# Kernel tuning notes

Hardware: AMD Instinct MI355X
Metric: run time of the kernel (lower is better)

The kernel has to match this reference:

```python
import jax, jax.numpy as jnp
import numpy as np

N = 8192
D_IN = 6       # dim(concat(node, centre)) = 3 + 3
D_OUT = 512    # output_size


def setup_inputs() -> dict:
    key = jax.random.key(0)
    ks = jax.random.split(key, 9)
    s_in = 1.0 / np.sqrt(D_IN)
    s_v = 1.0 / np.sqrt(2 * D_OUT)
    return {
        "nodes": jax.random.normal(ks[0], (N, 3), dtype=jnp.float32),
        "centre": jax.random.normal(ks[1], (1, 3), dtype=jnp.float32),
        "Wq": jax.random.uniform(ks[2], (D_OUT, D_IN), jnp.float32, -s_in, s_in),
        "bq": jax.random.uniform(ks[3], (D_OUT,), jnp.float32, -s_in, s_in),
        "Wk": jax.random.uniform(ks[4], (D_OUT, D_IN), jnp.float32, -s_in, s_in),
        "bk": jax.random.uniform(ks[5], (D_OUT,), jnp.float32, -s_in, s_in),
        "Wv": jax.random.uniform(ks[6], (D_OUT, 2 * D_OUT), jnp.float32, -s_v, s_v),
        "bv": jax.random.uniform(ks[7], (D_OUT,), jnp.float32, -s_v, s_v),
    }


def reference(nodes, centre, Wq, bq, Wk, bk, Wv, bv):
    n = nodes.shape[0]
    d = Wv.shape[0]
    # x = concat(nodes, broadcast centre)  -> [N, 6]
    x = jnp.concatenate([nodes, jnp.broadcast_to(centre, (n, centre.shape[1]))], axis=1)
    keys = x @ Wk.T + bk          # [N, D]
    queries = x @ Wq.T + bq       # [N, D]
    attn = jax.nn.softmax(keys @ queries.T, axis=1)  # [N, N], rows sum to 1
    # values(concat(queries, keys[n])) decomposes linearly:
    #   V[n, m] = queries[m] @ Wv_q.T + keys[n] @ Wv_k.T + bv
    # so out[n] = attn[n] @ (queries @ Wv_q.T) + keys[n] @ Wv_k.T + bv
    Wv_q = Wv[:, :d]
    Wv_k = Wv[:, d:]
    out = attn @ (queries @ Wv_q.T) + keys @ Wv_k.T + bv
    return keys + out
```

## Files before the change

### kernel.cpp

```cpp
#include <hip/hip_runtime.h>

#define N_NODES 8192
#define DOUT    512
#define LOG2E   1.4426950408889634f
#define SQRT3   1.7320508075688772f

__device__ __forceinline__ float exp2_raw(float x) {
    float r;
    asm("v_exp_f32 %0, %1" : "=v"(r) : "v"(x));
    return r;
}


__global__ __launch_bounds__(128) void k2_tables_aux(
    const float* __restrict__ nodes, const float* __restrict__ centre,
    const float* __restrict__ Wq, const float* __restrict__ bq,
    const float* __restrict__ Wk, const float* __restrict__ bk,
    const float* __restrict__ Wv, const float* __restrict__ bv,
    float* __restrict__ T, float* __restrict__ aux)
{
    __shared__ float red[16];
    const int r = blockIdx.x, tid = threadIdx.x, lane = tid & 63, wv = tid >> 6;
    const float c0 = centre[0], c1 = centre[1], c2 = centre[2];

    if (r < 512) {
        const float* wvq = Wv + (size_t)r * 1024;
        const float* wvk = wvq + 512;

        float m0=0.f,m1=0.f,m2=0.f,uc=0.f,r0=0.f,r1=0.f,r2=0.f,rc=0.f;
        #pragma unroll
        for (int it = 0; it < 4; ++it) {
            int s = it*128 + tid;
            float a = wvq[s];
            float b = wvk[s];
            const float2* wk2 = (const float2*)(Wk + s*6);
            const float2* wq2 = (const float2*)(Wq + s*6);
            float2 k01 = wk2[0], k23 = wk2[1], k45 = wk2[2];
            float2 q01 = wq2[0], q23 = wq2[1], q45 = wq2[2];
            float kcs = fmaf(k23.y, c0, fmaf(k45.x, c1, fmaf(k45.y, c2, bk[s])));
            float us  = fmaf(q23.y, c0, fmaf(q45.x, c1, fmaf(q45.y, c2, bq[s])));
            m0 = fmaf(a, q01.x, m0);
            m1 = fmaf(a, q01.y, m1);
            m2 = fmaf(a, q23.x, m2);
            uc = fmaf(a, us, uc);
            r0 = fmaf(b, k01.x, r0);
            r1 = fmaf(b, k01.y, r1);
            r2 = fmaf(b, k23.x, r2);
            rc = fmaf(b, kcs, rc);
        }
        #pragma unroll
        for (int off = 32; off; off >>= 1) {
            m0 += __shfl_xor(m0, off); m1 += __shfl_xor(m1, off);
            m2 += __shfl_xor(m2, off); uc += __shfl_xor(uc, off);
            r0 += __shfl_xor(r0, off); r1 += __shfl_xor(r1, off);
            r2 += __shfl_xor(r2, off); rc += __shfl_xor(rc, off);
        }
        if (lane == 0) {
            float* q = red + wv*8;
            q[0]=m0; q[1]=m1; q[2]=m2; q[3]=uc; q[4]=r0; q[5]=r1; q[6]=r2; q[7]=rc;
        }
        __syncthreads();
        if (tid == 0) {
            float kcr = fmaf(Wk[r*6+3], c0, fmaf(Wk[r*6+4], c1,
                        fmaf(Wk[r*6+5], c2, bk[r])));
            T[r*8+0] = Wk[r*6+0] + red[4] + red[12];
            T[r*8+1] = Wk[r*6+1] + red[5] + red[13];
            T[r*8+2] = Wk[r*6+2] + red[6] + red[14];
            T[r*8+3] = kcr + red[7] + red[15] + red[3] + red[11] + bv[r];
            T[r*8+4] = red[0] + red[8];
            T[r*8+5] = red[1] + red[9];
            T[r*8+6] = red[2] + red[10];
            T[r*8+7] = 0.f;
        }
    } else if (r < 524) {
        const int o = r - 512;
        float acc = 0.f;
        if (o < 9) {
            int a = o / 3, b = o - a*3;
            #pragma unroll
            for (int it = 0; it < 4; ++it) {
                int s = it*128 + tid;
                acc = fmaf(Wq[s*6+a], Wk[s*6+b], acc);
            }
        } else {
            int a = o - 9;
            #pragma unroll
            for (int it = 0; it < 4; ++it) {
                int s = it*128 + tid;
                float kc = fmaf(Wk[s*6+3], c0, fmaf(Wk[s*6+4], c1,
                           fmaf(Wk[s*6+5], c2, bk[s])));
                acc = fmaf(Wq[s*6+a], kc, acc);
            }
        }
        #pragma unroll
        for (int off = 32; off; off >>= 1) acc += __shfl_xor(acc, off);
        if (lane == 0) red[wv] = acc;
        __syncthreads();
        if (tid == 0) aux[o] = (red[0] + red[1]) * LOG2E;
    } else {
        const int b = r - 524;
        const float4* src = (const float4*)nodes + (size_t)b * 768;
        float m = 0.f;
        #pragma unroll
        for (int it = 0; it < 6; ++it) {
            float4 v = src[it*128 + tid];
            m = fmaxf(m, fmaxf(fmaxf(fabsf(v.x), fabsf(v.y)),
                               fmaxf(fabsf(v.z), fabsf(v.w))));
        }
        #pragma unroll
        for (int off = 32; off; off >>= 1) m = fmaxf(m, __shfl_xor(m, off));
        if (lane == 0) red[wv] = m;
        __syncthreads();
        if (tid == 0) aux[12 + b] = fmaxf(red[0], red[1]);
    }
}


__device__ __forceinline__ void stage_load(const float4* __restrict__ src, int tid,
                                           float4 v[4][3]) {
    #pragma unroll
    for (int k = 0; k < 4; ++k) {
        int t = k*256 + tid;
        v[k][0] = src[t*3+0];
        v[k][1] = src[t*3+1];
        v[k][2] = src[t*3+2];
    }
}

__device__ __forceinline__ void stage_write(float* __restrict__ lds, int tid,
                                            float4 v[4][3]) {
    #pragma unroll
    for (int k = 0; k < 4; ++k) {
        int t = k*256 + tid;
        float4 a = v[k][0], b = v[k][1], c = v[k][2];
        *(float4*)&lds[        t*4] = make_float4(a.x, a.w, b.z, c.y);
        *(float4*)&lds[4096 +  t*4] = make_float4(a.y, b.x, b.w, c.z);
        *(float4*)&lds[8192 +  t*4] = make_float4(a.z, b.y, c.x, c.w);
    }
}

__device__ __forceinline__ void attn_tile(const float* __restrict__ lds, int lane,
    const float vx[4], const float vy[4], const float vz[4], const float bb[4],
    float S[4], float ax[4], float ay[4], float az[4])
{
    #pragma unroll 2
    for (int it = 0; it < 16; ++it) {
        int jj = it*256 + lane*4;
        float4 X = *(const float4*)&lds[jj];
        float4 Y = *(const float4*)&lds[4096 + jj];
        float4 Z = *(const float4*)&lds[8192 + jj];
        #pragma unroll
        for (int q = 0; q < 4; ++q) {
            float a0 = fmaf(vx[q],X.x, fmaf(vy[q],Y.x, fmaf(vz[q],Z.x, bb[q])));
            float a1 = fmaf(vx[q],X.y, fmaf(vy[q],Y.y, fmaf(vz[q],Z.y, bb[q])));
            float a2 = fmaf(vx[q],X.z, fmaf(vy[q],Y.z, fmaf(vz[q],Z.z, bb[q])));
            float a3 = fmaf(vx[q],X.w, fmaf(vy[q],Y.w, fmaf(vz[q],Z.w, bb[q])));
            float e0 = exp2_raw(a0);
            float e1 = exp2_raw(a1);
            float e2 = exp2_raw(a2);
            float e3 = exp2_raw(a3);
            S[q] += e0; ax[q]=fmaf(e0,X.x,ax[q]); ay[q]=fmaf(e0,Y.x,ay[q]); az[q]=fmaf(e0,Z.x,az[q]);
            S[q] += e1; ax[q]=fmaf(e1,X.y,ax[q]); ay[q]=fmaf(e1,Y.y,ay[q]); az[q]=fmaf(e1,Z.y,az[q]);
            S[q] += e2; ax[q]=fmaf(e2,X.z,ax[q]); ay[q]=fmaf(e2,Y.z,ay[q]); az[q]=fmaf(e2,Z.z,az[q]);
            S[q] += e3; ax[q]=fmaf(e3,X.w,ax[q]); ay[q]=fmaf(e3,Y.w,ay[q]); az[q]=fmaf(e3,Z.w,az[q]);
        }
    }
}

__global__ __launch_bounds__(256, 2) void k3_attn(
    const float* __restrict__ nodes,
    const float* __restrict__ aux, const float* __restrict__ T,
    float* __restrict__ out)
{
    __shared__ float lds[12288];
    const int tid = threadIdx.x, lane = tid & 63, wv = tid >> 6;
    const int ibase = (blockIdx.x * 4 + wv) * 4;

    const float G00=aux[0],G01=aux[1],G02=aux[2];
    const float G10=aux[3],G11=aux[4],G12=aux[5];
    const float G20=aux[6],G21=aux[7],G22=aux[8];
    const float g0=aux[9],g1=aux[10],g2=aux[11];
    float C = aux[12];
    #pragma unroll
    for (int b = 1; b < 8; ++b) C = fmaxf(C, aux[12+b]);
    const float Nbound = SQRT3 * C;

    float nx_[4], ny_[4], nz_[4], vx[4], vy[4], vz[4], bb[4];
    float S[4], ax[4], ay[4], az[4];
    #pragma unroll
    for (int q = 0; q < 4; ++q) {
        int i = ibase + q;
        float x = nodes[3*i], y = nodes[3*i+1], z = nodes[3*i+2];
        nx_[q]=x; ny_[q]=y; nz_[q]=z;
        float a = fmaf(G00,x, fmaf(G01,y, fmaf(G02,z, g0)));
        float b = fmaf(G10,x, fmaf(G11,y, fmaf(G12,z, g1)));
        float c = fmaf(G20,x, fmaf(G21,y, fmaf(G22,z, g2)));
        vx[q]=a; vy[q]=b; vz[q]=c;
        bb[q] = -sqrtf(fmaf(a,a, fmaf(b,b, c*c))) * Nbound;
        S[q]=0.f; ax[q]=0.f; ay[q]=0.f; az[q]=0.f;
    }

    float4 s0[4][3], s1[4][3];
    stage_load((const float4*)nodes, tid, s0);
    stage_write(lds, tid, s0);
    stage_load((const float4*)(nodes + 12288), tid, s1);
    __syncthreads();
    attn_tile(lds, lane, vx, vy, vz, bb, S, ax, ay, az);
    __syncthreads();
    stage_write(lds, tid, s1);
    __syncthreads();
    attn_tile(lds, lane, vx, vy, vz, bb, S, ax, ay, az);

    #pragma unroll
    for (int q = 0; q < 4; ++q) {
        #pragma unroll
        for (int off = 32; off; off >>= 1) {
            S[q]  += __shfl_xor(S[q],  off);
            ax[q] += __shfl_xor(ax[q], off);
            ay[q] += __shfl_xor(ay[q], off);
            az[q] += __shfl_xor(az[q], off);
        }
        float inv = 1.f / fmaxf(S[q], 1e-35f);
        ax[q] *= inv; ay[q] *= inv; az[q] *= inv;
    }

    const float4* T4 = (const float4*)T;
    #pragma unroll
    for (int t = 0; t < 4; ++t) {
        int d0 = t*128 + lane*2;
        float4 A0 = T4[2*d0+0], B0 = T4[2*d0+1];
        float4 A1 = T4[2*d0+2], B1 = T4[2*d0+3];
        #pragma unroll
        for (int q = 0; q < 4; ++q) {
            float v0 = fmaf(A0.x,nx_[q], fmaf(A0.y,ny_[q], fmaf(A0.z,nz_[q],
                       fmaf(B0.x,ax[q], fmaf(B0.y,ay[q], fmaf(B0.z,az[q], A0.w))))));
            float v1 = fmaf(A1.x,nx_[q], fmaf(A1.y,ny_[q], fmaf(A1.z,nz_[q],
                       fmaf(B1.x,ax[q], fmaf(B1.y,ay[q], fmaf(B1.z,az[q], A1.w))))));
            *(float2*)(out + (size_t)(ibase+q)*DOUT + d0) = make_float2(v0, v1);
        }
    }
}

extern "C" void kernel_launch(void* const* d_in, const int* in_sizes, int n_in,
                              void* d_out, int out_size, void* d_ws, size_t ws_size,
                              hipStream_t stream) {
    const float* nodes  = (const float*)d_in[0];
    const float* centre = (const float*)d_in[1];
    const float* Wq     = (const float*)d_in[2];
    const float* bq     = (const float*)d_in[3];
    const float* Wk     = (const float*)d_in[4];
    const float* bk     = (const float*)d_in[5];
    const float* Wv     = (const float*)d_in[6];
    const float* bv     = (const float*)d_in[7];

    float* ws  = (float*)(((uintptr_t)d_ws + 255) & ~(uintptr_t)255);
    float* aux = ws;
    float* T   = ws + 32;
    float* out = (float*)d_out;

    hipLaunchKernelGGL(k2_tables_aux, dim3(532), dim3(128), 0, stream,
                       nodes, centre, Wq, bq, Wk, bk, Wv, bv, T, aux);
    hipLaunchKernelGGL(k3_attn,       dim3(512), dim3(256), 0, stream,
                       nodes, aux, T, out);
}
```

Measured before the change: 96.53 us.

## Move Wv table build into main kernel and overlap it via flag sync

The 512-row T-table computation (Wv contractions) moves out of the small pre-kernel into the first 128 blocks of the main attention kernel, one wave per row with float4 loads. The pre-kernel now computes only the Gram/aux terms and node max over 20 blocks. Attention blocks run their softmax tile loop concurrently and spin on an agent-scope atomic counter before the output projection that needs T. The aim is to take the heavy table build off the critical path. It adds a spin-wait that assumes the producer blocks get scheduled (forward progress), and occupancy hint rises to 3.

```diff
diff --git a/kernel.cpp b/kernel.cpp
--- a/kernel.cpp
+++ b/kernel.cpp
@@ -12,106 +12,58 @@
 }
 
 
-__global__ __launch_bounds__(128) void k2_tables_aux(
+__global__ __launch_bounds__(256) void kA_aux(
     const float* __restrict__ nodes, const float* __restrict__ centre,
-    const float* __restrict__ Wq, const float* __restrict__ bq,
-    const float* __restrict__ Wk, const float* __restrict__ bk,
-    const float* __restrict__ Wv, const float* __restrict__ bv,
-    float* __restrict__ T, float* __restrict__ aux)
+    const float* __restrict__ Wq, const float* __restrict__ Wk,
+    const float* __restrict__ bk,
+    float* __restrict__ aux, unsigned* __restrict__ flagT)
 {
-    __shared__ float red[16];
-    const int r = blockIdx.x, tid = threadIdx.x, lane = tid & 63, wv = tid >> 6;
+    __shared__ float red[4];
+    const int tid = threadIdx.x, lane = tid & 63, wv = tid >> 6;
+    const int b = blockIdx.x;
+    if (b == 0 && tid == 0) *flagT = 0u;
     const float c0 = centre[0], c1 = centre[1], c2 = centre[2];
 
-    if (r < 512) {
-        const float* wvq = Wv + (size_t)r * 1024;
-        const float* wvk = wvq + 512;
-
-        float m0=0.f,m1=0.f,m2=0.f,uc=0.f,r0=0.f,r1=0.f,r2=0.f,rc=0.f;
-        #pragma unroll
-        for (int it = 0; it < 4; ++it) {
-            int s = it*128 + tid;
-            float a = wvq[s];
-            float b = wvk[s];
-            const float2* wk2 = (const float2*)(Wk + s*6);
-            const float2* wq2 = (const float2*)(Wq + s*6);
-            float2 k01 = wk2[0], k23 = wk2[1], k45 = wk2[2];
-            float2 q01 = wq2[0], q23 = wq2[1], q45 = wq2[2];
-            float kcs = fmaf(k23.y, c0, fmaf(k45.x, c1, fmaf(k45.y, c2, bk[s])));
-            float us  = fmaf(q23.y, c0, fmaf(q45.x, c1, fmaf(q45.y, c2, bq[s])));
-            m0 = fmaf(a, q01.x, m0);
-            m1 = fmaf(a, q01.y, m1);
-            m2 = fmaf(a, q23.x, m2);
-            uc = fmaf(a, us, uc);
-            r0 = fmaf(b, k01.x, r0);
-            r1 = fmaf(b, k01.y, r1);
-            r2 = fmaf(b, k23.x, r2);
-            rc = fmaf(b, kcs, rc);
-        }
-        #pragma unroll
-        for (int off = 32; off; off >>= 1) {
-            m0 += __shfl_xor(m0, off); m1 += __shfl_xor(m1, off);
-            m2 += __shfl_xor(m2, off); uc += __shfl_xor(uc, off);
-            r0 += __shfl_xor(r0, off); r1 += __shfl_xor(r1, off);
-            r2 += __shfl_xor(r2, off); rc += __shfl_xor(rc, off);
-        }
-        if (lane == 0) {
-            float* q = red + wv*8;
-            q[0]=m0; q[1]=m1; q[2]=m2; q[3]=uc; q[4]=r0; q[5]=r1; q[6]=r2; q[7]=rc;
-        }
+    if (b < 8) {
+        const float4* src = (const float4*)nodes + (size_t)b * 768;
+        float m = 0.f;
+        #pragma unroll
+        for (int i = 0; i < 3; ++i) {
+            float4 v = src[tid + 256*i];
+            m = fmaxf(m, fmaxf(fmaxf(fabsf(v.x), fabsf(v.y)),
+                               fmaxf(fabsf(v.z), fabsf(v.w))));
+        }
+        #pragma unroll
+        for (int off = 32; off; off >>= 1) m = fmaxf(m, __shfl_xor(m, off));
+        if (lane == 0) red[wv] = m;
         __syncthreads();
-        if (tid == 0) {
-            float kcr = fmaf(Wk[r*6+3], c0, fmaf(Wk[r*6+4], c1,
-                        fmaf(Wk[r*6+5], c2, bk[r])));
-            T[r*8+0] = Wk[r*6+0] + red[4] + red[12];
-            T[r*8+1] = Wk[r*6+1] + red[5] + red[13];
-            T[r*8+2] = Wk[r*6+2] + red[6] + red[14];
-            T[r*8+3] = kcr + red[7] + red[15] + red[3] + red[11] + bv[r];
-            T[r*8+4] = red[0] + red[8];
-            T[r*8+5] = red[1] + red[9];
-            T[r*8+6] = red[2] + red[10];
-            T[r*8+7] = 0.f;
-        }
-    } else if (r < 524) {
-        const int o = r - 512;
+        if (tid == 0)
+            aux[12 + b] = fmaxf(fmaxf(red[0], red[1]), fmaxf(red[2], red[3]));
+    } else {
+        const int o = b - 8;
         float acc = 0.f;
         if (o < 9) {
-            int a = o / 3, b = o - a*3;
-            #pragma unroll
-            for (int it = 0; it < 4; ++it) {
-                int s = it*128 + tid;
-                acc = fmaf(Wq[s*6+a], Wk[s*6+b], acc);
+            int ra = o / 3, cb = o - ra*3;
+            #pragma unroll
+            for (int it = 0; it < 2; ++it) {
+                int s = it*256 + tid;
+                acc = fmaf(Wq[s*6+ra], Wk[s*6+cb], acc);
             }
         } else {
-            int a = o - 9;
-            #pragma unroll
-            for (int it = 0; it < 4; ++it) {
-                int s = it*128 + tid;
+            int ra = o - 9;
+            #pragma unroll
+            for (int it = 0; it < 2; ++it) {
+                int s = it*256 + tid;
                 float kc = fmaf(Wk[s*6+3], c0, fmaf(Wk[s*6+4], c1,
                            fmaf(Wk[s*6+5], c2, bk[s])));
-                acc = fmaf(Wq[s*6+a], kc, acc);
+                acc = fmaf(Wq[s*6+ra], kc, acc);
             }
         }
         #pragma unroll
         for (int off = 32; off; off >>= 1) acc += __shfl_xor(acc, off);
         if (lane == 0) red[wv] = acc;
         __syncthreads();
-        if (tid == 0) aux[o] = (red[0] + red[1]) * LOG2E;
-    } else {
-        const int b = r - 524;
-        const float4* src = (const float4*)nodes + (size_t)b * 768;
-        float m = 0.f;
-        #pragma unroll
-        for (int it = 0; it < 6; ++it) {
-            float4 v = src[it*128 + tid];
-            m = fmaxf(m, fmaxf(fmaxf(fabsf(v.x), fabsf(v.y)),
-                               fmaxf(fabsf(v.z), fabsf(v.w))));
-        }
-        #pragma unroll
-        for (int off = 32; off; off >>= 1) m = fmaxf(m, __shfl_xor(m, off));
-        if (lane == 0) red[wv] = m;
-        __syncthreads();
-        if (tid == 0) aux[12 + b] = fmaxf(red[0], red[1]);
+        if (tid == 0) aux[o] = (red[0]+red[1]+red[2]+red[3]) * LOG2E;
     }
 }
 
@@ -167,14 +119,81 @@
     }
 }
 
-__global__ __launch_bounds__(256, 2) void k3_attn(
-    const float* __restrict__ nodes,
-    const float* __restrict__ aux, const float* __restrict__ T,
-    float* __restrict__ out)
+__global__ __launch_bounds__(256, 3) void kB_main(
+    const float* __restrict__ nodes, const float* __restrict__ centre,
+    const float* __restrict__ Wq, const float* __restrict__ bq,
+    const float* __restrict__ Wk, const float* __restrict__ bk,
+    const float* __restrict__ Wv, const float* __restrict__ bv,
+    const float* __restrict__ aux, float* __restrict__ T,
+    unsigned* __restrict__ flagT, float* __restrict__ out)
 {
     __shared__ float lds[12288];
     const int tid = threadIdx.x, lane = tid & 63, wv = tid >> 6;
-    const int ibase = (blockIdx.x * 4 + wv) * 4;
+
+    if (blockIdx.x < 128) {
+        const int r = blockIdx.x*4 + wv;
+        const float c0 = centre[0], c1 = centre[1], c2 = centre[2];
+        const float* wvq = Wv + (size_t)r * 1024;
+        float m0=0.f,m1=0.f,m2=0.f,uc=0.f,r0=0.f,r1=0.f,r2=0.f,rc=0.f;
+        const int s0 = lane*8;
+        #pragma unroll
+        for (int h = 0; h < 2; ++h) {
+            const int sb = s0 + h*4;
+            float4 a4 = *(const float4*)(wvq + sb);
+            float4 b4 = *(const float4*)(wvq + 512 + sb);
+            float4 q_[6], k_[6];
+            #pragma unroll
+            for (int j = 0; j < 6; ++j) {
+                q_[j] = ((const float4*)(Wq + sb*6))[j];
+                k_[j] = ((const float4*)(Wk + sb*6))[j];
+            }
+            float4 bq4 = *(const float4*)(bq + sb);
+            float4 bk4 = *(const float4*)(bk + sb);
+            const float* qf = (const float*)q_;
+            const float* kf = (const float*)k_;
+            const float* af = (const float*)&a4;
+            const float* bf = (const float*)&b4;
+            const float* bqf = (const float*)&bq4;
+            const float* bkf = (const float*)&bk4;
+            #pragma unroll
+            for (int i = 0; i < 4; ++i) {
+                float a = af[i], w = bf[i];
+                float kcs = fmaf(kf[i*6+3], c0, fmaf(kf[i*6+4], c1,
+                            fmaf(kf[i*6+5], c2, bkf[i])));
+                float us  = fmaf(qf[i*6+3], c0, fmaf(qf[i*6+4], c1,
+                            fmaf(qf[i*6+5], c2, bqf[i])));
+                m0 = fmaf(a, qf[i*6+0], m0);
+                m1 = fmaf(a, qf[i*6+1], m1);
+                m2 = fmaf(a, qf[i*6+2], m2);
+                uc = fmaf(a, us, uc);
+                r0 = fmaf(w, kf[i*6+0], r0);
+                r1 = fmaf(w, kf[i*6+1], r1);
+                r2 = fmaf(w, kf[i*6+2], r2);
+                rc = fmaf(w, kcs, rc);
+            }
+        }
+        #pragma unroll
+        for (int off = 32; off; off >>= 1) {
+            m0 += __shfl_xor(m0, off); m1 += __shfl_xor(m1, off);
+            m2 += __shfl_xor(m2, off); uc += __shfl_xor(uc, off);
+            r0 += __shfl_xor(r0, off); r1 += __shfl_xor(r1, off);
+            r2 += __shfl_xor(r2, off); rc += __shfl_xor(rc, off);
+        }
+        if (lane == 0) {
+            float kcr = fmaf(Wk[r*6+3], c0, fmaf(Wk[r*6+4], c1,
+                        fmaf(Wk[r*6+5], c2, bk[r])));
+            T[r*8+0] = Wk[r*6+0] + r0;
+            T[r*8+1] = Wk[r*6+1] + r1;
+            T[r*8+2] = Wk[r*6+2] + r2;
+            T[r*8+3] = kcr + rc + uc + bv[r];
+            T[r*8+4] = m0; T[r*8+5] = m1; T[r*8+6] = m2; T[r*8+7] = 0.f;
+            __hip_atomic_fetch_add(flagT, 1u, __ATOMIC_RELEASE,
+                                   __HIP_MEMORY_SCOPE_AGENT);
+        }
+        return;
+    }
+
+    const int ibase = ((blockIdx.x - 128) * 4 + wv) * 4;
 
     const float G00=aux[0],G01=aux[1],G02=aux[2];
     const float G10=aux[3],G11=aux[4],G12=aux[5];
@@ -223,6 +242,10 @@
         float inv = 1.f / fmaxf(S[q], 1e-35f);
         ax[q] *= inv; ay[q] *= inv; az[q] *= inv;
     }
+
+    while (__hip_atomic_load(flagT, __ATOMIC_ACQUIRE,
+                             __HIP_MEMORY_SCOPE_AGENT) < 512u)
+        __builtin_amdgcn_s_sleep(2);
 
     const float4* T4 = (const float4*)T;
     #pragma unroll
@@ -253,13 +276,14 @@
     const float* Wv     = (const float*)d_in[6];
     const float* bv     = (const float*)d_in[7];
 
-    float* ws  = (float*)(((uintptr_t)d_ws + 255) & ~(uintptr_t)255);
-    float* aux = ws;
-    float* T   = ws + 32;
-    float* out = (float*)d_out;
-
-    hipLaunchKernelGGL(k2_tables_aux, dim3(532), dim3(128), 0, stream,
-                       nodes, centre, Wq, bq, Wk, bk, Wv, bv, T, aux);
-    hipLaunchKernelGGL(k3_attn,       dim3(512), dim3(256), 0, stream,
-                       nodes, aux, T, out);
-}
+    float* ws   = (float*)(((uintptr_t)d_ws + 255) & ~(uintptr_t)255);
+    float* aux  = ws;
+    unsigned* flagT = (unsigned*)(ws + 32);
+    float* T    = ws + 64;
+    float* out  = (float*)d_out;
+
+    hipLaunchKernelGGL(kA_aux, dim3(20), dim3(256), 0, stream,
+                       nodes, centre, Wq, Wk, bk, aux, flagT);
+    hipLaunchKernelGGL(kB_main, dim3(640), dim3(256), 0, stream,
+                       nodes, centre, Wq, bq, Wk, bk, Wv, bv, aux, T, flagT, out);
+}
```

New measurement: 123.9 us. 1.28x slower.

## Stage projected Wq/Wk rows in LDS and compute one table row per wave

Applied to the files above, without the earlier changes.

The table kernel now has each 256-thread block precompute the reduced Wq/Wk rows (first three columns plus the centre-folded bias term) into shared memory once. Each of its four waves then computes one row of T from LDS, which removes the repeated global gathers of Wk/Wq per row and the cross-wave reduction. The grid shrinks from 532 small blocks to 148 larger ones, and the aux and max-norm blocks are remapped to match. The cost is redundant LDS staging in every block, and the change only affects the small prologue kernel ahead of the attention kernel.

```diff
diff --git a/kernel.cpp b/kernel.cpp
--- a/kernel.cpp
+++ b/kernel.cpp
@@ -12,41 +12,47 @@
 }
 
 
-__global__ __launch_bounds__(128) void k2_tables_aux(
+__global__ __launch_bounds__(256) void k1_tables(
     const float* __restrict__ nodes, const float* __restrict__ centre,
     const float* __restrict__ Wq, const float* __restrict__ bq,
     const float* __restrict__ Wk, const float* __restrict__ bk,
     const float* __restrict__ Wv, const float* __restrict__ bv,
     float* __restrict__ T, float* __restrict__ aux)
 {
-    __shared__ float red[16];
-    const int r = blockIdx.x, tid = threadIdx.x, lane = tid & 63, wv = tid >> 6;
+    __shared__ float4 Bq_l[512];
+    __shared__ float4 Bk_l[512];
+    __shared__ float red[4];
+    const int tid = threadIdx.x, lane = tid & 63, wv_ = tid >> 6;
     const float c0 = centre[0], c1 = centre[1], c2 = centre[2];
 
-    if (r < 512) {
+    if (blockIdx.x < 128) {
+        for (int t = tid; t < 512; t += 256) {
+            const float2* wk2 = (const float2*)(Wk + t*6);
+            const float2* wq2 = (const float2*)(Wq + t*6);
+            float2 k01 = wk2[0], k23 = wk2[1], k45 = wk2[2];
+            float2 q01 = wq2[0], q23 = wq2[1], q45 = wq2[2];
+            float kc = fmaf(k23.y, c0, fmaf(k45.x, c1, fmaf(k45.y, c2, bk[t])));
+            float u  = fmaf(q23.y, c0, fmaf(q45.x, c1, fmaf(q45.y, c2, bq[t])));
+            Bk_l[t] = make_float4(k01.x, k01.y, k23.x, kc);
+            Bq_l[t] = make_float4(q01.x, q01.y, q23.x, u);
+        }
+        __syncthreads();
+
+        const int r = blockIdx.x*4 + wv_;
         const float* wvq = Wv + (size_t)r * 1024;
         const float* wvk = wvq + 512;
-
         float m0=0.f,m1=0.f,m2=0.f,uc=0.f,r0=0.f,r1=0.f,r2=0.f,rc=0.f;
         #pragma unroll
-        for (int it = 0; it < 4; ++it) {
-            int s = it*128 + tid;
+        for (int i = 0; i < 8; ++i) {
+            int s = i*64 + lane;
             float a = wvq[s];
             float b = wvk[s];
-            const float2* wk2 = (const float2*)(Wk + s*6);
-            const float2* wq2 = (const float2*)(Wq + s*6);
-            float2 k01 = wk2[0], k23 = wk2[1], k45 = wk2[2];
-            float2 q01 = wq2[0], q23 = wq2[1], q45 = wq2[2];
-            float kcs = fmaf(k23.y, c0, fmaf(k45.x, c1, fmaf(k45.y, c2, bk[s])));
-            float us  = fmaf(q23.y, c0, fmaf(q45.x, c1, fmaf(q45.y, c2, bq[s])));
-            m0 = fmaf(a, q01.x, m0);
-            m1 = fmaf(a, q01.y, m1);
-            m2 = fmaf(a, q23.x, m2);
-            uc = fmaf(a, us, uc);
-            r0 = fmaf(b, k01.x, r0);
-            r1 = fmaf(b, k01.y, r1);
-            r2 = fmaf(b, k23.x, r2);
-            rc = fmaf(b, kcs, rc);
+            float4 q4 = Bq_l[s];
+            float4 k4 = Bk_l[s];
+            m0 = fmaf(a, q4.x, m0); m1 = fmaf(a, q4.y, m1);
+            m2 = fmaf(a, q4.z, m2); uc = fmaf(a, q4.w, uc);
+            r0 = fmaf(b, k4.x, r0); r1 = fmaf(b, k4.y, r1);
+            r2 = fmaf(b, k4.z, r2); rc = fmaf(b, k4.w, rc);
         }
         #pragma unroll
         for (int off = 32; off; off >>= 1) {
@@ -56,62 +62,54 @@
             r2 += __shfl_xor(r2, off); rc += __shfl_xor(rc, off);
         }
         if (lane == 0) {
-            float* q = red + wv*8;
-            q[0]=m0; q[1]=m1; q[2]=m2; q[3]=uc; q[4]=r0; q[5]=r1; q[6]=r2; q[7]=rc;
-        }
+            float4 kr = Bk_l[r];
+            T[r*8+0] = kr.x + r0;
+            T[r*8+1] = kr.y + r1;
+            T[r*8+2] = kr.z + r2;
+            T[r*8+3] = kr.w + rc + uc + bv[r];
+            T[r*8+4] = m0; T[r*8+5] = m1; T[r*8+6] = m2; T[r*8+7] = 0.f;
+        }
+    } else if (blockIdx.x < 136) {
+        const int b = blockIdx.x - 128;
+        const float4* src = (const float4*)nodes + (size_t)b * 768;
+        float m = 0.f;
+        #pragma unroll
+        for (int i = 0; i < 3; ++i) {
+            float4 v = src[tid + 256*i];
+            m = fmaxf(m, fmaxf(fmaxf(fabsf(v.x), fabsf(v.y)),
+                               fmaxf(fabsf(v.z), fabsf(v.w))));
+        }
+        #pragma unroll
+        for (int off = 32; off; off >>= 1) m = fmaxf(m, __shfl_xor(m, off));
+        if (lane == 0) red[wv_] = m;
         __syncthreads();
-        if (tid == 0) {
-            float kcr = fmaf(Wk[r*6+3], c0, fmaf(Wk[r*6+4], c1,
-                        fmaf(Wk[r*6+5], c2, bk[r])));
-            T[r*8+0] = Wk[r*6+0] + red[4] + red[12];
-            T[r*8+1] = Wk[r*6+1] + red[5] + red[13];
-            T[r*8+2] = Wk[r*6+2] + red[6] + red[14];
-            T[r*8+3] = kcr + red[7] + red[15] + red[3] + red[11] + bv[r];
-            T[r*8+4] = red[0] + red[8];
-            T[r*8+5] = red[1] + red[9];
-            T[r*8+6] = red[2] + red[10];
-            T[r*8+7] = 0.f;
-        }
-    } else if (r < 524) {
-        const int o = r - 512;
+        if (tid == 0)
+            aux[12 + b] = fmaxf(fmaxf(red[0], red[1]), fmaxf(red[2], red[3]));
+    } else {
+        const int o = blockIdx.x - 136;
         float acc = 0.f;
         if (o < 9) {
-            int a = o / 3, b = o - a*3;
+            int ra = o / 3, cb = o - ra*3;
             #pragma unroll
-            for (int it = 0; it < 4; ++it) {
-                int s = it*128 + tid;
-                acc = fmaf(Wq[s*6+a], Wk[s*6+b], acc);
+            for (int it = 0; it < 2; ++it) {
+                int s = it*256 + tid;
+                acc = fmaf(Wq[s*6+ra], Wk[s*6+cb], acc);
             }
         } else {
-            int a = o - 9;
+            int ra = o - 9;
             #pragma unroll
-            for (int it = 0; it < 4; ++it) {
-                int s = it*128 + tid;
+            for (int it = 0; it < 2; ++it) {
+                int s = it*256 + tid;
                 float kc = fmaf(Wk[s*6+3], c0, fmaf(Wk[s*6+4], c1,
                            fmaf(Wk[s*6+5], c2, bk[s])));
-                acc = fmaf(Wq[s*6+a], kc, acc);
+                acc = fmaf(Wq[s*6+ra], kc, acc);
             }
         }
         #pragma unroll
         for (int off = 32; off; off >>= 1) acc += __shfl_xor(acc, off);
-        if (lane == 0) red[wv] = acc;
+        if (lane == 0) red[wv_] = acc;
         __syncthreads();
-        if (tid == 0) aux[o] = (red[0] + red[1]) * LOG2E;
-    } else {
-        const int b = r - 524;
-        const float4* src = (const float4*)nodes + (size_t)b * 768;
-        float m = 0.f;
-        #pragma unroll
-        for (int it = 0; it < 6; ++it) {
-            float4 v = src[it*128 + tid];
-            m = fmaxf(m, fmaxf(fmaxf(fabsf(v.x), fabsf(v.y)),
-                               fmaxf(fabsf(v.z), fabsf(v.w))));
-        }
-        #pragma unroll
-        for (int off = 32; off; off >>= 1) m = fmaxf(m, __shfl_xor(m, off));
-        if (lane == 0) red[wv] = m;
-        __syncthreads();
-        if (tid == 0) aux[12 + b] = fmaxf(red[0], red[1]);
+        if (tid == 0) aux[o] = (red[0]+red[1]+red[2]+red[3]) * LOG2E;
     }
 }
 
@@ -200,14 +198,14 @@
         S[q]=0.f; ax[q]=0.f; ay[q]=0.f; az[q]=0.f;
     }
 
-    float4 s0[4][3], s1[4][3];
-    stage_load((const float4*)nodes, tid, s0);
-    stage_write(lds, tid, s0);
-    stage_load((const float4*)(nodes + 12288), tid, s1);
+    float4 s0v[4][3], s1v[4][3];
+    stage_load((const float4*)nodes, tid, s0v);
+    stage_write(lds, tid, s0v);
+    stage_load((const float4*)(nodes + 12288), tid, s1v);
     __syncthreads();
     attn_tile(lds, lane, vx, vy, vz, bb, S, ax, ay, az);
     __syncthreads();
-    stage_write(lds, tid, s1);
+    stage_write(lds, tid, s1v);
     __syncthreads();
     attn_tile(lds, lane, vx, vy, vz, bb, S, ax, ay, az);
 
@@ -255,11 +253,11 @@
 
     float* ws  = (float*)(((uintptr_t)d_ws + 255) & ~(uintptr_t)255);
     float* aux = ws;
-    float* T   = ws + 32;
+    float* T   = ws + 64;
     float* out = (float*)d_out;
 
-    hipLaunchKernelGGL(k2_tables_aux, dim3(532), dim3(128), 0, stream,
+    hipLaunchKernelGGL(k1_tables, dim3(148), dim3(256), 0, stream,
                        nodes, centre, Wq, bq, Wk, bk, Wv, bv, T, aux);
-    hipLaunchKernelGGL(k3_attn,       dim3(512), dim3(256), 0, stream,
+    hipLaunchKernelGGL(k3_attn,   dim3(512), dim3(256), 0, stream,
                        nodes, aux, T, out);
 }
```

Measured after the change: 96.52 us, median of 2. About the same (-0.0%).
